# Performance work log

Measured on AMD Instinct MI355X. Metric: run time of the kernel, lower is better.

Reference implementation:

```python
import jax, jax.numpy as jnp
import numpy as np

H = 16      # numHeads (== numKeyValueHeads since keyValueHeadsPerHead=1)
D = 128     # headDim


def setup_inputs() -> dict:
    key = jax.random.key(0)
    k1, k2, k3 = jax.random.split(key, 3)
    B, S, dim = 2, 2048, 2048
    x = jax.random.normal(k1, (B, S, dim), dtype=jnp.float32)
    # qkvProj: Linear(dim -> (H + 2*H)*D) without bias; torch Linear weight is [out, in]
    Wqkv = jax.random.normal(k2, ((H + 2 * H) * D, dim), dtype=jnp.float32) * 0.02
    # outProj: Linear(H*D -> dim) without bias
    Wout = jax.random.normal(k3, (dim, H * D), dtype=jnp.float32) * 0.02
    return {"x": x, "Wqkv": Wqkv, "Wout": Wout}


def reference(x, Wqkv, Wout):
    B, S, _ = x.shape
    qkv = jnp.einsum('bsd,ed->bse', x, Wqkv)           # [B, S, 3*H*D]
    qkv = qkv.reshape(B, S, 3 * H, D)
    q = qkv[:, :, :H]                                  # [B, S, H, D]
    k = qkv[:, :, H:2 * H]                             # [B, S, H, D]
    v = qkv[:, :, 2 * H:]                              # [B, S, H, D]
    # explicit QK^T / sqrt(d), softmax in fp32, then @ V (keyValueHeadsPerHead=1
    # collapses the group axis, leaving standard per-head attention)
    logits = jnp.einsum('bqhd,bkhd->bhqk', q, k) * (D ** -0.5)
    w = jax.nn.softmax(logits.astype(jnp.float32), axis=-1).astype(logits.dtype)
    out = jnp.einsum('bhqk,bkhd->bqhd', w, v).reshape(B, S, H * D)
    return jnp.einsum('bse,de->bsd', out, Wout)        # outProj
```

## Files before the change

### kernel.cpp

```cpp
#include <hip/hip_runtime.h>

typedef __bf16 bf16x8 __attribute__((ext_vector_type(8)));
typedef _Float16 f16;
typedef f16 f16x8 __attribute__((ext_vector_type(8)));
typedef float f32x4 __attribute__((ext_vector_type(4)));
typedef unsigned short u16;
typedef u16 u16x4 __attribute__((ext_vector_type(4)));

__device__ __forceinline__ u16 f2bf(float f) {
  unsigned u = __builtin_bit_cast(unsigned, f);
  u += 0x7FFFu + ((u >> 16) & 1u);
  return (u16)(u >> 16);
}

#define GLDS16(g, l) __builtin_amdgcn_global_load_lds(                     \
    (const __attribute__((address_space(1))) unsigned int*)(g),            \
    (__attribute__((address_space(3))) unsigned int*)(l), 16, 0, 0)

__device__ __forceinline__ f32x4 mfma16(bf16x8 a, bf16x8 b, f32x4 c) {
  return __builtin_amdgcn_mfma_f32_16x16x32_bf16(a, b, c, 0, 0, 0);
}
__device__ __forceinline__ f32x4 mfma16h(f16x8 a, f16x8 b, f32x4 c) {
  return __builtin_amdgcn_mfma_f32_16x16x32_f16(a, b, c, 0, 0, 0);
}

__global__ void cvt_all(const float* __restrict__ x, const float* __restrict__ wqkv,
                        const float* __restrict__ wout, u16* __restrict__ xb,
                        u16* __restrict__ wqkvb, u16* __restrict__ woutb, float qscale) {
  int idx = blockIdx.x * blockDim.x + threadIdx.x;
  int stride = gridDim.x * blockDim.x;
  for (int i = idx; i < 6291456; i += stride) {
    const float* src; u16* dst; int j; float sc = 1.0f;
    if (i < 2097152)      { src = x;    dst = xb;    j = i; }
    else if (i < 5242880) { j = i - 2097152; src = wqkv; dst = wqkvb;
                            if (j < 1048576) sc = qscale; }
    else                  { j = i - 5242880; src = wout; dst = woutb; }
    float4 v = ((const float4*)src)[j];
    u16x4 o = { f2bf(v.x * sc), f2bf(v.y * sc), f2bf(v.z * sc), f2bf(v.w * sc) };
    ((u16x4*)dst)[j] = o;
  }
}

__global__ __launch_bounds__(256, 2) void gemm1_qkv(
    const u16* __restrict__ A, const u16* __restrict__ B,
    u16* __restrict__ QK, u16* __restrict__ VT) {
  __shared__ __align__(16) u16 LA[2][8192];
  __shared__ __align__(16) u16 LB[2][12288];
  constexpr int K = 2048;
  const int t = threadIdx.x, lane = t & 63, w = t >> 6;
  const int wm = w >> 1, wn = w & 1;
  const int l15 = lane & 15, lg = lane >> 4;
  const int l7 = l15 & 7;

  const int bid = blockIdx.x;
  const int wg = (bid & 7) * 128 + (bid >> 3);
  const int bx = wg & 31, by = wg >> 5;
  const int m0 = by * 128, n0 = bx * 192;
  const int ks0 = bid & 31;

  const int srow = t >> 3;
  const int schunk = (t & 7) ^ (srow & 7);
  const u16* ga = A + (size_t)(m0 + srow) * K + schunk * 8;
  const u16* gb = B + (size_t)(n0 + srow) * K + schunk * 8;

  f32x4 acc[4][6] = {};

#define STG_A(ch, kt, bfi)                                                 \
    GLDS16(ga + (kt) * 64 + (size_t)(ch) * 32 * K, &LA[bfi][(ch) * 2048] + t * 8)
#define STG_B(ch, kt, bfi)                                                 \
    GLDS16(gb + (kt) * 64 + (size_t)(ch) * 32 * K, &LB[bfi][(ch) * 2048] + t * 8)

  STG_A(0, ks0, 0); STG_A(2, ks0, 0); STG_B(0, ks0, 0);
  STG_B(1, ks0, 0); STG_B(3, ks0, 0); STG_B(4, ks0, 0);
  STG_B(2, ks0, 0); STG_B(5, ks0, 0);
  STG_A(1, ks0, 0); STG_A(3, ks0, 0);
  asm volatile("s_waitcnt vmcnt(4)" ::: "memory");
  __builtin_amdgcn_s_barrier();

#pragma unroll 1
  for (int T = 0; T < 32; ++T) {
    const int p = T & 1, np = p ^ 1;
    const bool st = (T < 31);
    const int ktn = (T + 1 + ks0) & 31;
    const u16* la = &LA[p][0];
    const u16* lb = &LB[p][0];
    bf16x8 aF[2][2], bLo[2][3], bHi[2][3];

#pragma unroll
    for (int kk = 0; kk < 2; ++kk) {
      const int cp = ((kk * 4 + lg) ^ l7) * 8;
#pragma unroll
      for (int i = 0; i < 2; ++i)
        aF[kk][i] = *(const bf16x8*)&la[(wm * 64 + i * 16 + l15) * 64 + cp];
#pragma unroll
      for (int j = 0; j < 3; ++j)
        bLo[kk][j] = *(const bf16x8*)&lb[(wn * 96 + j * 16 + l15) * 64 + cp];
    }
    if (st) {
      STG_A(0, ktn, np); STG_A(2, ktn, np); STG_B(0, ktn, np);
      asm volatile("s_waitcnt vmcnt(5)" ::: "memory");
    } else {
      asm volatile("s_waitcnt vmcnt(2)" ::: "memory");
    }
    __builtin_amdgcn_s_barrier();
    asm volatile("s_waitcnt lgkmcnt(0)" ::: "memory");
    __builtin_amdgcn_sched_barrier(0);
    __builtin_amdgcn_s_setprio(1);
#pragma unroll
    for (int i = 0; i < 2; ++i)
#pragma unroll
      for (int j = 0; j < 3; ++j)
#pragma unroll
        for (int kk = 0; kk < 2; ++kk)
          acc[i][j] = mfma16(aF[kk][i], bLo[kk][j], acc[i][j]);
    __builtin_amdgcn_s_setprio(0);
    __builtin_amdgcn_s_barrier();

#pragma unroll
    for (int kk = 0; kk < 2; ++kk) {
      const int cp = ((kk * 4 + lg) ^ l7) * 8;
#pragma unroll
      for (int j = 0; j < 3; ++j)
        bHi[kk][j] = *(const bf16x8*)&lb[(wn * 96 + 48 + j * 16 + l15) * 64 + cp];
    }
    if (st) {
      STG_B(1, ktn, np); STG_B(3, ktn, np); STG_B(4, ktn, np);
      asm volatile("s_waitcnt vmcnt(6)" ::: "memory");
    } else {
      asm volatile("s_waitcnt vmcnt(0)" ::: "memory");
    }
    __builtin_amdgcn_s_barrier();
    asm volatile("s_waitcnt lgkmcnt(0)" ::: "memory");
    __builtin_amdgcn_sched_barrier(0);
    __builtin_amdgcn_s_setprio(1);
#pragma unroll
    for (int i = 0; i < 2; ++i)
#pragma unroll
      for (int j = 0; j < 3; ++j)
#pragma unroll
        for (int kk = 0; kk < 2; ++kk)
          acc[i][3 + j] = mfma16(aF[kk][i], bHi[kk][j], acc[i][3 + j]);
    __builtin_amdgcn_s_setprio(0);
    __builtin_amdgcn_s_barrier();

#pragma unroll
    for (int kk = 0; kk < 2; ++kk) {
      const int cp = ((kk * 4 + lg) ^ l7) * 8;
#pragma unroll
      for (int i = 0; i < 2; ++i)
        aF[kk][i] = *(const bf16x8*)&la[(wm * 64 + 32 + i * 16 + l15) * 64 + cp];
    }
    if (st) { STG_B(2, ktn, np); STG_B(5, ktn, np); }
    __builtin_amdgcn_s_barrier();
    asm volatile("s_waitcnt lgkmcnt(0)" ::: "memory");
    __builtin_amdgcn_sched_barrier(0);
    __builtin_amdgcn_s_setprio(1);
#pragma unroll
    for (int i = 0; i < 2; ++i)
#pragma unroll
      for (int j = 0; j < 3; ++j)
#pragma unroll
        for (int kk = 0; kk < 2; ++kk)
          acc[2 + i][j] = mfma16(aF[kk][i], bLo[kk][j], acc[2 + i][j]);
    __builtin_amdgcn_s_setprio(0);
    __builtin_amdgcn_s_barrier();

    if (st) {
      STG_A(1, ktn, np); STG_A(3, ktn, np);
      asm volatile("s_waitcnt vmcnt(4)" ::: "memory");
    }
    __builtin_amdgcn_s_barrier();
    __builtin_amdgcn_s_setprio(1);
#pragma unroll
    for (int i = 0; i < 2; ++i)
#pragma unroll
      for (int j = 0; j < 3; ++j)
#pragma unroll
        for (int kk = 0; kk < 2; ++kk)
          acc[2 + i][3 + j] = mfma16(aF[kk][i], bHi[kk][j], acc[2 + i][3 + j]);
    __builtin_amdgcn_s_setprio(0);
    __builtin_amdgcn_s_barrier();
  }
#undef STG_A
#undef STG_B

  const int rb = m0 + wm * 64 + lg * 4;
  const int cb = n0 + wn * 96 + l15;
#pragma unroll
  for (int i = 0; i < 4; ++i) {
#pragma unroll
    for (int j = 0; j < 6; ++j) {
      const int row0 = rb + i * 16;
      const int col = cb + j * 16;
      if (col < 4096) {
#pragma unroll
        for (int jj = 0; jj < 4; ++jj)
          QK[(size_t)(row0 + jj) * 4096 + col] = f2bf(acc[i][j][jj]);
      } else {
        const int vcol = col - 4096;
        const int bb = row0 >> 11, s = row0 & 2047;
        auto h0 = __builtin_amdgcn_cvt_pkrtz(acc[i][j][0], acc[i][j][1]);
        auto h1 = __builtin_amdgcn_cvt_pkrtz(acc[i][j][2], acc[i][j][3]);
        uint2 pk;
        pk.x = __builtin_bit_cast(unsigned, h0);
        pk.y = __builtin_bit_cast(unsigned, h1);
        *(uint2*)&VT[((size_t)bb * 2048 + vcol) * 2048 + s] = pk;
      }
    }
  }
}

__global__ __launch_bounds__(256, 2) void gemm2_out(
    const u16* __restrict__ A, const u16* __restrict__ B,
    float* __restrict__ C) {
  __shared__ __align__(16) u16 LA[2][8192];
  __shared__ __align__(16) u16 LB[2][8192];
  constexpr int K = 2048, N = 2048;
  const int t = threadIdx.x, lane = t & 63, w = t >> 6;
  const int wm = w >> 1, wn = w & 1;
  const int l15 = lane & 15, lg = lane >> 4;
  const int l7 = l15 & 7;

  const int bid = blockIdx.x;
  const int wg = (bid & 7) * 64 + (bid >> 3);
  const int bx = wg & 15, by = wg >> 4;
  const int m0 = by * 128, n0 = bx * 128;
  const int ks0 = bid & 31;

  const int srow = t >> 3;
  const int schunk = (t & 7) ^ (srow & 7);
  const u16* ga = A + (size_t)(m0 + srow) * K + schunk * 8;
  const u16* gb = B + (size_t)(n0 + srow) * K + schunk * 8;

  f32x4 acc[4][4] = {};

#define STG_A(ch, kt, bfi)                                                 \
    GLDS16(ga + (kt) * 64 + (size_t)(ch) * 32 * K, &LA[bfi][(ch) * 2048] + t * 8)
#define STG_B(ch, kt, bfi)                                                 \
    GLDS16(gb + (kt) * 64 + (size_t)(ch) * 32 * K, &LB[bfi][(ch) * 2048] + t * 8)

  STG_A(0, ks0, 0); STG_A(2, ks0, 0); STG_B(0, ks0, 0); STG_B(2, ks0, 0);
  STG_B(1, ks0, 0); STG_B(3, ks0, 0);
  STG_A(1, ks0, 0); STG_A(3, ks0, 0);
  asm volatile("s_waitcnt vmcnt(4)" ::: "memory");
  __builtin_amdgcn_s_barrier();

#pragma unroll 1
  for (int T = 0; T < 32; ++T) {
    const int p = T & 1, np = p ^ 1;
    const bool st = (T < 31);
    const int ktn = (T + 1 + ks0) & 31;
    const u16* la = &LA[p][0];
    const u16* lb = &LB[p][0];
    bf16x8 aF[2][2], bLo[2][2], bHi[2][2];

#pragma unroll
    for (int kk = 0; kk < 2; ++kk) {
      const int cp = ((kk * 4 + lg) ^ l7) * 8;
#pragma unroll
      for (int i = 0; i < 2; ++i) {
        aF[kk][i]  = *(const bf16x8*)&la[(wm * 64 + i * 16 + l15) * 64 + cp];
        bLo[kk][i] = *(const bf16x8*)&lb[(wn * 64 + i * 16 + l15) * 64 + cp];
      }
    }
    if (st) {
      STG_A(0, ktn, np); STG_A(2, ktn, np);
      asm volatile("s_waitcnt vmcnt(4)" ::: "memory");
    } else {
      asm volatile("s_waitcnt vmcnt(2)" ::: "memory");
    }
    __builtin_amdgcn_s_barrier();
    asm volatile("s_waitcnt lgkmcnt(0)" ::: "memory");
    __builtin_amdgcn_sched_barrier(0);
    __builtin_amdgcn_s_setprio(1);
#pragma unroll
    for (int i = 0; i < 2; ++i)
#pragma unroll
      for (int j = 0; j < 2; ++j)
#pragma unroll
        for (int kk = 0; kk < 2; ++kk)
          acc[i][j] = mfma16(aF[kk][i], bLo[kk][j], acc[i][j]);
    __builtin_amdgcn_s_setprio(0);
    __builtin_amdgcn_s_barrier();

#pragma unroll
    for (int kk = 0; kk < 2; ++kk) {
      const int cp = ((kk * 4 + lg) ^ l7) * 8;
#pragma unroll
      for (int j = 0; j < 2; ++j)
        bHi[kk][j] = *(const bf16x8*)&lb[(wn * 64 + 32 + j * 16 + l15) * 64 + cp];
    }
    if (st) {
      STG_B(0, ktn, np); STG_B(2, ktn, np);
      asm volatile("s_waitcnt vmcnt(4)" ::: "memory");
    } else {
      asm volatile("s_waitcnt vmcnt(0)" ::: "memory");
    }
    __builtin_amdgcn_s_barrier();
    asm volatile("s_waitcnt lgkmcnt(0)" ::: "memory");
    __builtin_amdgcn_sched_barrier(0);
    __builtin_amdgcn_s_setprio(1);
#pragma unroll
    for (int i = 0; i < 2; ++i)
#pragma unroll
      for (int j = 0; j < 2; ++j)
#pragma unroll
        for (int kk = 0; kk < 2; ++kk)
          acc[i][2 + j] = mfma16(aF[kk][i], bHi[kk][j], acc[i][2 + j]);
    __builtin_amdgcn_s_setprio(0);
    __builtin_amdgcn_s_barrier();

#pragma unroll
    for (int kk = 0; kk < 2; ++kk) {
      const int cp = ((kk * 4 + lg) ^ l7) * 8;
#pragma unroll
      for (int i = 0; i < 2; ++i)
        aF[kk][i] = *(const bf16x8*)&la[(wm * 64 + 32 + i * 16 + l15) * 64 + cp];
    }
    if (st) { STG_B(1, ktn, np); STG_B(3, ktn, np); }
    __builtin_amdgcn_s_barrier();
    asm volatile("s_waitcnt lgkmcnt(0)" ::: "memory");
    __builtin_amdgcn_sched_barrier(0);
    __builtin_amdgcn_s_setprio(1);
#pragma unroll
    for (int i = 0; i < 2; ++i)
#pragma unroll
      for (int j = 0; j < 2; ++j)
#pragma unroll
        for (int kk = 0; kk < 2; ++kk)
          acc[2 + i][j] = mfma16(aF[kk][i], bLo[kk][j], acc[2 + i][j]);
    __builtin_amdgcn_s_setprio(0);
    __builtin_amdgcn_s_barrier();

    if (st) {
      STG_A(1, ktn, np); STG_A(3, ktn, np);
      asm volatile("s_waitcnt vmcnt(4)" ::: "memory");
    }
    __builtin_amdgcn_s_barrier();
    __builtin_amdgcn_s_setprio(1);
#pragma unroll
    for (int i = 0; i < 2; ++i)
#pragma unroll
      for (int j = 0; j < 2; ++j)
#pragma unroll
        for (int kk = 0; kk < 2; ++kk)
          acc[2 + i][2 + j] = mfma16(aF[kk][i], bHi[kk][j], acc[2 + i][2 + j]);
    __builtin_amdgcn_s_setprio(0);
    __builtin_amdgcn_s_barrier();
  }
#undef STG_A
#undef STG_B

  const int rb = m0 + wm * 64 + lg * 4;
  const int cb = n0 + wn * 64 + l15;
#pragma unroll
  for (int i = 0; i < 4; ++i)
#pragma unroll
    for (int j = 0; j < 4; ++j) {
      const int row0 = rb + i * 16;
      const int col = cb + j * 16;
#pragma unroll
      for (int jj = 0; jj < 4; ++jj)
        C[(size_t)(row0 + jj) * N + col] = acc[i][j][jj];
    }
}

#define PSTRIDE 72
__global__ __launch_bounds__(512, 1) void attn_fwd(
    const u16* __restrict__ qk, const u16* __restrict__ vt, u16* __restrict__ aout) {
  __shared__ __align__(16) u16 Ks[2][64 * 128];
  __shared__ __align__(16) u16 Vs[2][128 * 64];
  __shared__ __align__(16) u16 Pl[8][32 * PSTRIDE];
  const int t = threadIdx.x, lane = t & 63, w = t >> 6;
  const int bh = blockIdx.x;
  const int b = bh >> 4, h = bh & 15;
  const int q0 = blockIdx.y * 256 + w * 32;
  const int l15 = lane & 15, lg = lane >> 4;

  const u16* qp = qk + (size_t)b * 2048 * 4096 + h * 128;
  const u16* kp = qp + 2048;
  const u16* vtp = vt + (size_t)(b * 16 + h) * 128 * 2048;
  u16* op = aout + (size_t)b * 2048 * 2048 + h * 128;

  int ksoff[2], vsoff[2];
#pragma unroll
  for (int rd = 0; rd < 2; ++rd) {
    const int r = rd * 32 + (t >> 4);
    const int c = (t & 15) ^ (r & 15);
    ksoff[rd] = r * 4096 + c * 8;
    const int rv = rd * 64 + (t >> 3);
    const int cv = (t & 7) ^ (rv & 7);
    vsoff[rd] = rv * 2048 + cv * 8;
  }

  bf16x8 qf[2][4];
#pragma unroll
  for (int mi = 0; mi < 2; ++mi)
#pragma unroll
    for (int kd = 0; kd < 4; ++kd)
      qf[mi][kd] = *(const bf16x8*)&qp[(size_t)(q0 + mi * 16 + l15) * 4096 + kd * 32 + lg * 8];

  f32x4 o[2][8] = {};
  f32x4 lacc[2] = {};
  const f16x8 onesf = {f16(1.f), f16(1.f), f16(1.f), f16(1.f),
                       f16(1.f), f16(1.f), f16(1.f), f16(1.f)};
  u16* pw = &Pl[w][0];

#pragma unroll
  for (int rd = 0; rd < 2; ++rd) {
    GLDS16(kp + ksoff[rd], &Ks[0][0] + rd * 4096 + t * 8);
    GLDS16(vtp + vsoff[rd], &Vs[0][0] + rd * 4096 + t * 8);
  }
  __syncthreads();

  auto tile = [&](const u16* ksb, const u16* vsb, u16* kpre, u16* vpre, int nextit) {
    if (nextit < 32) {
      const size_t kt1 = (size_t)nextit * 64;
#pragma unroll
      for (int rd = 0; rd < 2; ++rd) {
        GLDS16(kp + kt1 * 4096 + ksoff[rd], kpre + rd * 4096 + t * 8);
        GLDS16(vtp + kt1 + vsoff[rd], vpre + rd * 4096 + t * 8);
      }
    }
    f32x4 sf[2][4];
    __builtin_amdgcn_s_setprio(1);
#pragma unroll
    for (int ni = 0; ni < 4; ++ni) {
      const int r = ni * 16 + l15;
      bf16x8 kf[4];
#pragma unroll
      for (int kd = 0; kd < 4; ++kd)
        kf[kd] = *(const bf16x8*)&ksb[r * 128 + (((kd * 4 + lg) ^ l15) * 8)];
#pragma unroll
      for (int mi = 0; mi < 2; ++mi) {
        f32x4 s = {0.f, 0.f, 0.f, 0.f};
        s = mfma16(kf[0], qf[mi][0], s);
        s = mfma16(kf[1], qf[mi][1], s);
        s = mfma16(kf[2], qf[mi][2], s);
        s = mfma16(kf[3], qf[mi][3], s);
        sf[mi][ni] = s;
      }
    }
    __builtin_amdgcn_s_setprio(0);

#pragma unroll
    for (int mi = 0; mi < 2; ++mi)
#pragma unroll
      for (int ni = 0; ni < 4; ++ni) {
        float p0 = exp2f(sf[mi][ni][0]);
        float p1 = exp2f(sf[mi][ni][1]);
        float p2 = exp2f(sf[mi][ni][2]);
        float p3 = exp2f(sf[mi][ni][3]);
        auto h0 = __builtin_amdgcn_cvt_pkrtz(p0, p1);
        auto h1 = __builtin_amdgcn_cvt_pkrtz(p2, p3);
        uint2 wv;
        wv.x = __builtin_bit_cast(unsigned, h0);
        wv.y = __builtin_bit_cast(unsigned, h1);
        *(uint2*)&pw[(mi * 16 + l15) * PSTRIDE + ni * 16 + lg * 4] = wv;
      }

    f16x8 pa[2][2];
#pragma unroll
    for (int mi = 0; mi < 2; ++mi)
#pragma unroll
      for (int ks = 0; ks < 2; ++ks)
        pa[mi][ks] = *(const f16x8*)&pw[(mi * 16 + l15) * PSTRIDE + ks * 32 + lg * 8];
    __builtin_amdgcn_s_setprio(1);
#pragma unroll
    for (int mi = 0; mi < 2; ++mi) {
      lacc[mi] = mfma16h(pa[mi][0], onesf, lacc[mi]);
      lacc[mi] = mfma16h(pa[mi][1], onesf, lacc[mi]);
    }
#pragma unroll
    for (int n2 = 0; n2 < 8; ++n2) {
      const int r = n2 * 16 + l15;
      f16x8 vf0 = *(const f16x8*)&vsb[r * 64 + (((0 * 4 + lg) ^ (l15 & 7)) * 8)];
      f16x8 vf1 = *(const f16x8*)&vsb[r * 64 + (((1 * 4 + lg) ^ (l15 & 7)) * 8)];
#pragma unroll
      for (int mi = 0; mi < 2; ++mi) {
        o[mi][n2] = mfma16h(pa[mi][0], vf0, o[mi][n2]);
        o[mi][n2] = mfma16h(pa[mi][1], vf1, o[mi][n2]);
      }
    }
    __builtin_amdgcn_s_setprio(0);
    __syncthreads();
  };

#pragma unroll 1
  for (int it = 0; it < 32; it += 2) {
    tile(&Ks[0][0], &Vs[0][0], &Ks[1][0], &Vs[1][0], it + 1);
    tile(&Ks[1][0], &Vs[1][0], &Ks[0][0], &Vs[0][0], it + 2);
  }

#pragma unroll
  for (int mi = 0; mi < 2; ++mi)
#pragma unroll
    for (int j = 0; j < 4; ++j) {
      float inv = 1.f / lacc[mi][j];
#pragma unroll
      for (int n2 = 0; n2 < 8; ++n2)
        op[(size_t)(q0 + mi * 16 + lg * 4 + j) * 2048 + n2 * 16 + l15] =
            f2bf(o[mi][n2][j] * inv);
    }
}

extern "C" void kernel_launch(void* const* d_in, const int* in_sizes, int n_in,
                              void* d_out, int out_size, void* d_ws, size_t ws_size,
                              hipStream_t stream) {
  const float* x    = (const float*)d_in[0];
  const float* Wqkv = (const float*)d_in[1];
  const float* Wout = (const float*)d_in[2];
  float* out = (float*)d_out;

  u16* ws = (u16*)d_ws;
  u16* xb    = ws;
  u16* wqkvb = ws + 8388608;
  u16* woutb = ws + 20971520;
  u16* qkbuf = ws + 25165824;
  u16* vtbuf = ws + 41943040;
  u16* aout  = xb;

  const float qscale = 0.08838834764831845f * 1.4426950408889634f;

  cvt_all<<<2048, 256, 0, stream>>>(x, Wqkv, Wout, xb, wqkvb, woutb, qscale);

  gemm1_qkv<<<1024, 256, 0, stream>>>(xb, wqkvb, qkbuf, vtbuf);
  attn_fwd<<<dim3(32, 8, 1), 512, 0, stream>>>(qkbuf, vtbuf, aout);
  gemm2_out<<<512, 256, 0, stream>>>(aout, woutb, out);
}
```

Baseline: 254.9 us.

## Replace 4-phase interleaved GEMM pipeline with simple full-tile double buffering

Both GEMM kernels drop the four-phase schedule that interleaved partial LDS reads, staged global-to-LDS loads and MFMA blocks with barriers between them. The new loop issues all loads for the next K tile at the top, waits on the current tile, reads all fragments, then runs every MFMA in one block. The per-block rotated K start offset (ks0) is also removed, so all blocks walk K in the same order. This cuts barriers and simplifies scheduling, but it gives up the fine-grained overlap of memory and MFMA work, holds more fragment registers at once, and may add DRAM or L2 contention now that blocks no longer stagger their K start.

```diff
diff --git a/kernel.cpp b/kernel.cpp
--- a/kernel.cpp
+++ b/kernel.cpp
@@ -56,7 +56,6 @@
   const int wg = (bid & 7) * 128 + (bid >> 3);
   const int bx = wg & 31, by = wg >> 5;
   const int m0 = by * 128, n0 = bx * 192;
-  const int ks0 = bid & 31;
 
   const int srow = t >> 3;
   const int schunk = (t & 7) ^ (srow & 7);
@@ -69,120 +68,81 @@
     GLDS16(ga + (kt) * 64 + (size_t)(ch) * 32 * K, &LA[bfi][(ch) * 2048] + t * 8)
 #define STG_B(ch, kt, bfi)                                                 \
     GLDS16(gb + (kt) * 64 + (size_t)(ch) * 32 * K, &LB[bfi][(ch) * 2048] + t * 8)
-
-  STG_A(0, ks0, 0); STG_A(2, ks0, 0); STG_B(0, ks0, 0);
-  STG_B(1, ks0, 0); STG_B(3, ks0, 0); STG_B(4, ks0, 0);
-  STG_B(2, ks0, 0); STG_B(5, ks0, 0);
-  STG_A(1, ks0, 0); STG_A(3, ks0, 0);
-  asm volatile("s_waitcnt vmcnt(4)" ::: "memory");
-  __builtin_amdgcn_s_barrier();
+#define STG_ALL(kt, bfi) do {                                              \
+    STG_A(0, kt, bfi); STG_A(1, kt, bfi); STG_A(2, kt, bfi); STG_A(3, kt, bfi); \
+    STG_B(0, kt, bfi); STG_B(1, kt, bfi); STG_B(2, kt, bfi);               \
+    STG_B(3, kt, bfi); STG_B(4, kt, bfi); STG_B(5, kt, bfi);               \
+  } while (0)
+
+  STG_ALL(0, 0);
 
 #pragma unroll 1
   for (int T = 0; T < 32; ++T) {
     const int p = T & 1, np = p ^ 1;
-    const bool st = (T < 31);
-    const int ktn = (T + 1 + ks0) & 31;
+    if (T < 31) {
+      STG_ALL(T + 1, np);
+      asm volatile("s_waitcnt vmcnt(10)" ::: "memory");
+    } else {
+      asm volatile("s_waitcnt vmcnt(0)" ::: "memory");
+    }
+    __builtin_amdgcn_s_barrier();
+
     const u16* la = &LA[p][0];
     const u16* lb = &LB[p][0];
-    bf16x8 aF[2][2], bLo[2][3], bHi[2][3];
-
+    bf16x8 aLo[2][2], aHi[2][2], bLo[2][3], bHi[2][3];
 #pragma unroll
     for (int kk = 0; kk < 2; ++kk) {
       const int cp = ((kk * 4 + lg) ^ l7) * 8;
 #pragma unroll
       for (int i = 0; i < 2; ++i)
-        aF[kk][i] = *(const bf16x8*)&la[(wm * 64 + i * 16 + l15) * 64 + cp];
+        aLo[kk][i] = *(const bf16x8*)&la[(wm * 64 + i * 16 + l15) * 64 + cp];
 #pragma unroll
       for (int j = 0; j < 3; ++j)
         bLo[kk][j] = *(const bf16x8*)&lb[(wn * 96 + j * 16 + l15) * 64 + cp];
-    }
-    if (st) {
-      STG_A(0, ktn, np); STG_A(2, ktn, np); STG_B(0, ktn, np);
-      asm volatile("s_waitcnt vmcnt(5)" ::: "memory");
-    } else {
-      asm volatile("s_waitcnt vmcnt(2)" ::: "memory");
-    }
-    __builtin_amdgcn_s_barrier();
+#pragma unroll
+      for (int j = 0; j < 3; ++j)
+        bHi[kk][j] = *(const bf16x8*)&lb[(wn * 96 + 48 + j * 16 + l15) * 64 + cp];
+#pragma unroll
+      for (int i = 0; i < 2; ++i)
+        aHi[kk][i] = *(const bf16x8*)&la[(wm * 64 + 32 + i * 16 + l15) * 64 + cp];
+    }
+    __builtin_amdgcn_s_setprio(1);
+#pragma unroll
+    for (int i = 0; i < 2; ++i)
+#pragma unroll
+      for (int j = 0; j < 3; ++j)
+#pragma unroll
+        for (int kk = 0; kk < 2; ++kk)
+          acc[i][j] = mfma16(aLo[kk][i], bLo[kk][j], acc[i][j]);
+#pragma unroll
+    for (int i = 0; i < 2; ++i)
+#pragma unroll
+      for (int j = 0; j < 3; ++j)
+#pragma unroll
+        for (int kk = 0; kk < 2; ++kk)
+          acc[i][3 + j] = mfma16(aLo[kk][i], bHi[kk][j], acc[i][3 + j]);
+#pragma unroll
+    for (int i = 0; i < 2; ++i)
+#pragma unroll
+      for (int j = 0; j < 3; ++j)
+#pragma unroll
+        for (int kk = 0; kk < 2; ++kk)
+          acc[2 + i][j] = mfma16(aHi[kk][i], bLo[kk][j], acc[2 + i][j]);
+#pragma unroll
+    for (int i = 0; i < 2; ++i)
+#pragma unroll
+      for (int j = 0; j < 3; ++j)
+#pragma unroll
+        for (int kk = 0; kk < 2; ++kk)
+          acc[2 + i][3 + j] = mfma16(aHi[kk][i], bHi[kk][j], acc[2 + i][3 + j]);
+    __builtin_amdgcn_s_setprio(0);
+
     asm volatile("s_waitcnt lgkmcnt(0)" ::: "memory");
-    __builtin_amdgcn_sched_barrier(0);
-    __builtin_amdgcn_s_setprio(1);
-#pragma unroll
-    for (int i = 0; i < 2; ++i)
-#pragma unroll
-      for (int j = 0; j < 3; ++j)
-#pragma unroll
-        for (int kk = 0; kk < 2; ++kk)
-          acc[i][j] = mfma16(aF[kk][i], bLo[kk][j], acc[i][j]);
-    __builtin_amdgcn_s_setprio(0);
-    __builtin_amdgcn_s_barrier();
-
-#pragma unroll
-    for (int kk = 0; kk < 2; ++kk) {
-      const int cp = ((kk * 4 + lg) ^ l7) * 8;
-#pragma unroll
-      for (int j = 0; j < 3; ++j)
-        bHi[kk][j] = *(const bf16x8*)&lb[(wn * 96 + 48 + j * 16 + l15) * 64 + cp];
-    }
-    if (st) {
-      STG_B(1, ktn, np); STG_B(3, ktn, np); STG_B(4, ktn, np);
-      asm volatile("s_waitcnt vmcnt(6)" ::: "memory");
-    } else {
-      asm volatile("s_waitcnt vmcnt(0)" ::: "memory");
-    }
-    __builtin_amdgcn_s_barrier();
-    asm volatile("s_waitcnt lgkmcnt(0)" ::: "memory");
-    __builtin_amdgcn_sched_barrier(0);
-    __builtin_amdgcn_s_setprio(1);
-#pragma unroll
-    for (int i = 0; i < 2; ++i)
-#pragma unroll
-      for (int j = 0; j < 3; ++j)
-#pragma unroll
-        for (int kk = 0; kk < 2; ++kk)
-          acc[i][3 + j] = mfma16(aF[kk][i], bHi[kk][j], acc[i][3 + j]);
-    __builtin_amdgcn_s_setprio(0);
-    __builtin_amdgcn_s_barrier();
-
-#pragma unroll
-    for (int kk = 0; kk < 2; ++kk) {
-      const int cp = ((kk * 4 + lg) ^ l7) * 8;
-#pragma unroll
-      for (int i = 0; i < 2; ++i)
-        aF[kk][i] = *(const bf16x8*)&la[(wm * 64 + 32 + i * 16 + l15) * 64 + cp];
-    }
-    if (st) { STG_B(2, ktn, np); STG_B(5, ktn, np); }
-    __builtin_amdgcn_s_barrier();
-    asm volatile("s_waitcnt lgkmcnt(0)" ::: "memory");
-    __builtin_amdgcn_sched_barrier(0);
-    __builtin_amdgcn_s_setprio(1);
-#pragma unroll
-    for (int i = 0; i < 2; ++i)
-#pragma unroll
-      for (int j = 0; j < 3; ++j)
-#pragma unroll
-        for (int kk = 0; kk < 2; ++kk)
-          acc[2 + i][j] = mfma16(aF[kk][i], bLo[kk][j], acc[2 + i][j]);
-    __builtin_amdgcn_s_setprio(0);
-    __builtin_amdgcn_s_barrier();
-
-    if (st) {
-      STG_A(1, ktn, np); STG_A(3, ktn, np);
-      asm volatile("s_waitcnt vmcnt(4)" ::: "memory");
-    }
-    __builtin_amdgcn_s_barrier();
-    __builtin_amdgcn_s_setprio(1);
-#pragma unroll
-    for (int i = 0; i < 2; ++i)
-#pragma unroll
-      for (int j = 0; j < 3; ++j)
-#pragma unroll
-        for (int kk = 0; kk < 2; ++kk)
-          acc[2 + i][3 + j] = mfma16(aF[kk][i], bHi[kk][j], acc[2 + i][3 + j]);
-    __builtin_amdgcn_s_setprio(0);
     __builtin_amdgcn_s_barrier();
   }
 #undef STG_A
 #undef STG_B
+#undef STG_ALL
 
   const int rb = m0 + wm * 64 + lg * 4;
   const int cb = n0 + wn * 96 + l15;
@@ -225,7 +185,6 @@
   const int wg = (bid & 7) * 64 + (bid >> 3);
   const int bx = wg & 15, by = wg >> 4;
   const int m0 = by * 128, n0 = bx * 128;
-  const int ks0 = bid & 31;
 
   const int srow = t >> 3;
   const int schunk = (t & 7) ^ (srow & 7);
@@ -238,118 +197,75 @@
     GLDS16(ga + (kt) * 64 + (size_t)(ch) * 32 * K, &LA[bfi][(ch) * 2048] + t * 8)
 #define STG_B(ch, kt, bfi)                                                 \
     GLDS16(gb + (kt) * 64 + (size_t)(ch) * 32 * K, &LB[bfi][(ch) * 2048] + t * 8)
-
-  STG_A(0, ks0, 0); STG_A(2, ks0, 0); STG_B(0, ks0, 0); STG_B(2, ks0, 0);
-  STG_B(1, ks0, 0); STG_B(3, ks0, 0);
-  STG_A(1, ks0, 0); STG_A(3, ks0, 0);
-  asm volatile("s_waitcnt vmcnt(4)" ::: "memory");
-  __builtin_amdgcn_s_barrier();
+#define STG_ALL(kt, bfi) do {                                              \
+    STG_A(0, kt, bfi); STG_A(1, kt, bfi); STG_A(2, kt, bfi); STG_A(3, kt, bfi); \
+    STG_B(0, kt, bfi); STG_B(1, kt, bfi); STG_B(2, kt, bfi); STG_B(3, kt, bfi); \
+  } while (0)
+
+  STG_ALL(0, 0);
 
 #pragma unroll 1
   for (int T = 0; T < 32; ++T) {
     const int p = T & 1, np = p ^ 1;
-    const bool st = (T < 31);
-    const int ktn = (T + 1 + ks0) & 31;
+    if (T < 31) {
+      STG_ALL(T + 1, np);
+      asm volatile("s_waitcnt vmcnt(8)" ::: "memory");
+    } else {
+      asm volatile("s_waitcnt vmcnt(0)" ::: "memory");
+    }
+    __builtin_amdgcn_s_barrier();
+
     const u16* la = &LA[p][0];
     const u16* lb = &LB[p][0];
-    bf16x8 aF[2][2], bLo[2][2], bHi[2][2];
-
+    bf16x8 aLo[2][2], aHi[2][2], bLo[2][2], bHi[2][2];
 #pragma unroll
     for (int kk = 0; kk < 2; ++kk) {
       const int cp = ((kk * 4 + lg) ^ l7) * 8;
 #pragma unroll
       for (int i = 0; i < 2; ++i) {
-        aF[kk][i]  = *(const bf16x8*)&la[(wm * 64 + i * 16 + l15) * 64 + cp];
+        aLo[kk][i] = *(const bf16x8*)&la[(wm * 64 + i * 16 + l15) * 64 + cp];
         bLo[kk][i] = *(const bf16x8*)&lb[(wn * 64 + i * 16 + l15) * 64 + cp];
-      }
-    }
-    if (st) {
-      STG_A(0, ktn, np); STG_A(2, ktn, np);
-      asm volatile("s_waitcnt vmcnt(4)" ::: "memory");
-    } else {
-      asm volatile("s_waitcnt vmcnt(2)" ::: "memory");
-    }
-    __builtin_amdgcn_s_barrier();
+        bHi[kk][i] = *(const bf16x8*)&lb[(wn * 64 + 32 + i * 16 + l15) * 64 + cp];
+        aHi[kk][i] = *(const bf16x8*)&la[(wm * 64 + 32 + i * 16 + l15) * 64 + cp];
+      }
+    }
+    __builtin_amdgcn_s_setprio(1);
+#pragma unroll
+    for (int i = 0; i < 2; ++i)
+#pragma unroll
+      for (int j = 0; j < 2; ++j)
+#pragma unroll
+        for (int kk = 0; kk < 2; ++kk)
+          acc[i][j] = mfma16(aLo[kk][i], bLo[kk][j], acc[i][j]);
+#pragma unroll
+    for (int i = 0; i < 2; ++i)
+#pragma unroll
+      for (int j = 0; j < 2; ++j)
+#pragma unroll
+        for (int kk = 0; kk < 2; ++kk)
+          acc[i][2 + j] = mfma16(aLo[kk][i], bHi[kk][j], acc[i][2 + j]);
+#pragma unroll
+    for (int i = 0; i < 2; ++i)
+#pragma unroll
+      for (int j = 0; j < 2; ++j)
+#pragma unroll
+        for (int kk = 0; kk < 2; ++kk)
+          acc[2 + i][j] = mfma16(aHi[kk][i], bLo[kk][j], acc[2 + i][j]);
+#pragma unroll
+    for (int i = 0; i < 2; ++i)
+#pragma unroll
+      for (int j = 0; j < 2; ++j)
+#pragma unroll
+        for (int kk = 0; kk < 2; ++kk)
+          acc[2 + i][2 + j] = mfma16(aHi[kk][i], bHi[kk][j], acc[2 + i][2 + j]);
+    __builtin_amdgcn_s_setprio(0);
+
     asm volatile("s_waitcnt lgkmcnt(0)" ::: "memory");
-    __builtin_amdgcn_sched_barrier(0);
-    __builtin_amdgcn_s_setprio(1);
-#pragma unroll
-    for (int i = 0; i < 2; ++i)
-#pragma unroll
-      for (int j = 0; j < 2; ++j)
-#pragma unroll
-        for (int kk = 0; kk < 2; ++kk)
-          acc[i][j] = mfma16(aF[kk][i], bLo[kk][j], acc[i][j]);
-    __builtin_amdgcn_s_setprio(0);
-    __builtin_amdgcn_s_barrier();
-
-#pragma unroll
-    for (int kk = 0; kk < 2; ++kk) {
-      const int cp = ((kk * 4 + lg) ^ l7) * 8;
-#pragma unroll
-      for (int j = 0; j < 2; ++j)
-        bHi[kk][j] = *(const bf16x8*)&lb[(wn * 64 + 32 + j * 16 + l15) * 64 + cp];
-    }
-    if (st) {
-      STG_B(0, ktn, np); STG_B(2, ktn, np);
-      asm volatile("s_waitcnt vmcnt(4)" ::: "memory");
-    } else {
-      asm volatile("s_waitcnt vmcnt(0)" ::: "memory");
-    }
-    __builtin_amdgcn_s_barrier();
-    asm volatile("s_waitcnt lgkmcnt(0)" ::: "memory");
-    __builtin_amdgcn_sched_barrier(0);
-    __builtin_amdgcn_s_setprio(1);
-#pragma unroll
-    for (int i = 0; i < 2; ++i)
-#pragma unroll
-      for (int j = 0; j < 2; ++j)
-#pragma unroll
-        for (int kk = 0; kk < 2; ++kk)
-          acc[i][2 + j] = mfma16(aF[kk][i], bHi[kk][j], acc[i][2 + j]);
-    __builtin_amdgcn_s_setprio(0);
-    __builtin_amdgcn_s_barrier();
-
-#pragma unroll
-    for (int kk = 0; kk < 2; ++kk) {
-      const int cp = ((kk * 4 + lg) ^ l7) * 8;
-#pragma unroll
-      for (int i = 0; i < 2; ++i)
-        aF[kk][i] = *(const bf16x8*)&la[(wm * 64 + 32 + i * 16 + l15) * 64 + cp];
-    }
-    if (st) { STG_B(1, ktn, np); STG_B(3, ktn, np); }
-    __builtin_amdgcn_s_barrier();
-    asm volatile("s_waitcnt lgkmcnt(0)" ::: "memory");
-    __builtin_amdgcn_sched_barrier(0);
-    __builtin_amdgcn_s_setprio(1);
-#pragma unroll
-    for (int i = 0; i < 2; ++i)
-#pragma unroll
-      for (int j = 0; j < 2; ++j)
-#pragma unroll
-        for (int kk = 0; kk < 2; ++kk)
-          acc[2 + i][j] = mfma16(aF[kk][i], bLo[kk][j], acc[2 + i][j]);
-    __builtin_amdgcn_s_setprio(0);
-    __builtin_amdgcn_s_barrier();
-
-    if (st) {
-      STG_A(1, ktn, np); STG_A(3, ktn, np);
-      asm volatile("s_waitcnt vmcnt(4)" ::: "memory");
-    }
-    __builtin_amdgcn_s_barrier();
-    __builtin_amdgcn_s_setprio(1);
-#pragma unroll
-    for (int i = 0; i < 2; ++i)
-#pragma unroll
-      for (int j = 0; j < 2; ++j)
-#pragma unroll
-        for (int kk = 0; kk < 2; ++kk)
-          acc[2 + i][2 + j] = mfma16(aF[kk][i], bHi[kk][j], acc[2 + i][2 + j]);
-    __builtin_amdgcn_s_setprio(0);
     __builtin_amdgcn_s_barrier();
   }
 #undef STG_A
 #undef STG_B
+#undef STG_ALL
 
   const int rb = m0 + wm * 64 + lg * 4;
   const int cb = n0 + wn * 64 + l15;
```

Result: faster. 244.9 us (median of 2 runs) (-3.9%).
